# Kernel optimization log

Measured on AMD Instinct MI355X. Metric: run time of the kernel, lower is better.

Reference implementation:

```python
import jax, jax.numpy as jnp
import numpy as np

EPS = 1e-6

def _ln(x):
    mu = jnp.mean(x, -1, keepdims=True)
    var = jnp.mean((x - mu) ** 2, -1, keepdims=True)
    return (x - mu) / jnp.sqrt(var + EPS)

def _mha(q_in, k_in, v_in, w, mask, h):
    # w: [4, d, d] = (Wq, Wk, Wv, Wo), stored as [in, out]
    b, sq, d = q_in.shape
    dk = d // h
    q = (q_in @ w[0]).reshape(b, sq, h, dk)
    k = (k_in @ w[1]).reshape(b, k_in.shape[1], h, dk)
    v = (v_in @ w[2]).reshape(b, v_in.shape[1], h, dk)
    scores = jnp.einsum('bqhd,bkhd->bhqk', q, k) / np.sqrt(dk).astype(q.dtype)
    if mask is not None:
        scores = jnp.where(mask, scores, jnp.asarray(-jnp.inf, scores.dtype))
    attn = jax.nn.softmax(scores, -1)
    out = jnp.einsum('bhqk,bkhd->bqhd', attn, v).reshape(b, sq, d)
    return out @ w[3]

def setup_inputs() -> dict:
    B, S, D, V, NL, ML = 8, 256, 1024, 32000, 6, 256
    ks = jax.random.split(jax.random.key(0), 8)
    sc = 0.02
    return {
        'memory': jax.random.normal(ks[0], (B, S, D), jnp.float32),
        'gold_tokens': jax.random.randint(ks[1], (B, ML), 0, V),
        'attn_w': jax.random.normal(ks[2], (NL, 2, 4, D, D), jnp.float32) * sc,
        'ffn_w1': jax.random.normal(ks[3], (NL, D, 4 * D), jnp.float32) * sc,
        'ffn_w2': jax.random.normal(ks[4], (NL, 4 * D, D), jnp.float32) * sc,
        'tok_emb': jax.random.normal(ks[5], (V, D - ML), jnp.float32) * sc,
        'sos': jax.random.normal(ks[6], (D,), jnp.float32),
        'gen_w': jax.random.normal(ks[7], (D, V), jnp.float32) * sc,
    }

def reference(memory, gold_tokens, attn_w, ffn_w1, ffn_w2, tok_emb, sos, gen_w):
    B = memory.shape[0]
    ML = gold_tokens.shape[1]          # max_length == decoder len
    NL = attn_w.shape[0]
    H = 8
    temperature = 1.0
    # embedding: token embed (dim d-ML) concat one-hot position (dim ML)
    dec_input = gold_tokens[:, :-1]                      # [B, ML-1]
    tok = tok_emb[dec_input]                             # [B, ML-1, D-ML]
    pos = jax.nn.one_hot(jnp.arange(ML - 1), ML, dtype=tok.dtype)  # [ML-1, ML]
    pos = jnp.broadcast_to(pos[None], (B, ML - 1, ML))
    emb = jnp.concatenate([tok, pos], -1)                # [B, ML-1, D]
    sos_tok = jnp.broadcast_to(sos[None, None, :], (B, 1, sos.shape[0]))
    x = jnp.concatenate([sos_tok, emb], 1)               # [B, ML, D]
    causal = jnp.tril(jnp.ones((ML, ML), bool))[None, None]  # True = keep
    for l in range(NL):
        h1 = _ln(x)
        x = x + _mha(h1, h1, h1, attn_w[l, 0], causal, H)       # self-attn
        x = x + _mha(_ln(x), memory, memory, attn_w[l, 1], None, H)  # cross-attn (raw memory keys/values)
        h2 = _ln(x)
        x = x + jax.nn.relu(h2 @ ffn_w1[l]) @ ffn_w2[l]
    logits = _ln(x) @ gen_w
    return jax.nn.log_softmax(logits / temperature, -1)
```

## Files before the change

### kernel.cpp

```cpp
#include <hip/hip_runtime.h>
#include <hip/hip_bf16.h>
#include <cstdint>
#include <cstddef>

using bf16 = __hip_bfloat16;
typedef __attribute__((ext_vector_type(8))) short bf16x8;
typedef __attribute__((ext_vector_type(4))) float f32x4;

#define DEV static __device__ __forceinline__

DEV unsigned short f2bf(float f) {
    bf16 h = __float2bfloat16(f);
    return __builtin_bit_cast(unsigned short, h);
}

typedef const __attribute__((address_space(1))) void* as1cv;
typedef __attribute__((address_space(3))) void* as3v;

DEV void load_lds16(const void* g, void* l) {
    __builtin_amdgcn_global_load_lds((as1cv)g, (as3v)l, 16, 0, 0);
}

template<int EPI>
__global__ __launch_bounds__(256)
void gemm_k(const bf16* __restrict__ Ag, const bf16* __restrict__ Bg,
            void* __restrict__ Cg,
            int Mdim, int Ndim, int Kdim,
            int lda, int ldb, int ldc,
            int Hdim, long aZ1, long aZ2, long bZ1, long bZ2,
            long cZ1, long cZ2, float scale,
            float* __restrict__ pp, const bf16* __restrict__ Ag2, int ySplitA)
{
    __shared__ __align__(16) char lds[65536];

    const int t = threadIdx.x;
    const int wave = t >> 6, lane = t & 63;
    const int wr = wave >> 1, wc = wave & 1;
    const int lo = lane & 15, hi = lane >> 4;

    const int bx2 = blockIdx.x, by2 = blockIdx.y;
    const int m0 = bx2 * 128, n0 = by2 * 128;
    const int z = blockIdx.z;
    const int z1 = z / Hdim, z2 = z - z1 * Hdim;

    const bf16* Abase = (by2 >= ySplitA) ? Ag2 : Ag;
    const bf16* A = Abase + (size_t)z1 * aZ1 + (size_t)z2 * aZ2;
    const bf16* B = Bg + (size_t)z1 * bZ1 + (size_t)z2 * bZ2;

    f32x4 acc[4][4];
#pragma unroll
    for (int m = 0; m < 4; ++m)
#pragma unroll
        for (int n = 0; n < 4; ++n)
            acc[m][n] = f32x4{0.f, 0.f, 0.f, 0.f};

    const int nk = Kdim >> 6;

    auto stage = [&](int kt, int buf) {
        const int k0 = kt << 6;
        char* dA = lds + buf * 32768;
        char* dB = dA + 16384;
#pragma unroll
        for (int i = 0; i < 4; ++i) {
            int u = i * 256 + t;
            int row = u >> 3;
            int cb = (u & 7) ^ (row & 7);
            load_lds16(A + (size_t)(m0 + row) * lda + (k0 + cb * 8),
                       dA + i * 4096 + wave * 1024);
        }
#pragma unroll
        for (int i = 0; i < 4; ++i) {
            int u = i * 256 + t;
            int row = u >> 3;
            int cb = (u & 7) ^ (row & 7);
            load_lds16(B + (size_t)(n0 + row) * ldb + (k0 + cb * 8),
                       dB + i * 4096 + wave * 1024);
        }
    };

    stage(0, 0);
    int cur = 0;
    for (int kt = 0; kt < nk; ++kt) {
        __syncthreads();
        if (kt + 1 < nk) stage(kt + 1, cur ^ 1);
        char* ldsA = lds + cur * 32768;
        char* ldsB = ldsA + 16384;
#pragma unroll
        for (int kk = 0; kk < 2; ++kk) {
            bf16x8 af[4], bfr[4];
#pragma unroll
            for (int m = 0; m < 4; ++m) {
                int row = wr * 64 + m * 16 + lo;
                int cbyte = ((kk << 6) + (hi << 4)) ^ ((row & 7) << 4);
                af[m] = *(const bf16x8*)(ldsA + row * 128 + cbyte);
            }
#pragma unroll
            for (int n = 0; n < 4; ++n) {
                int row = wc * 64 + n * 16 + lo;
                int cbyte = ((kk << 6) + (hi << 4)) ^ ((row & 7) << 4);
                bfr[n] = *(const bf16x8*)(ldsB + row * 128 + cbyte);
            }
#pragma unroll
            for (int m = 0; m < 4; ++m)
#pragma unroll
                for (int n = 0; n < 4; ++n)
                    acc[m][n] = __builtin_amdgcn_mfma_f32_16x16x32_bf16(
                        af[m], bfr[n], acc[m][n], 0, 0, 0);
        }
        cur ^= 1;
    }

    const int rb = hi << 2;
    if (EPI == 0 || EPI == 1) {
        unsigned short* C = (unsigned short*)Cg + (size_t)z1 * cZ1 + (size_t)z2 * cZ2;
#pragma unroll
        for (int m = 0; m < 4; ++m)
#pragma unroll
            for (int n = 0; n < 4; ++n)
#pragma unroll
                for (int r = 0; r < 4; ++r) {
                    int row = m0 + wr * 64 + m * 16 + rb + r;
                    int col = n0 + wc * 64 + n * 16 + lo;
                    float v = acc[m][n][r];
                    if (EPI == 1) v = fmaxf(v, 0.f);
                    C[(size_t)row * ldc + col] = f2bf(v);
                }
    } else if (EPI == 5) {
        float* C = (float*)Cg + (size_t)z1 * cZ1 + (size_t)z2 * cZ2;
#pragma unroll
        for (int m = 0; m < 4; ++m)
#pragma unroll
            for (int n = 0; n < 4; ++n)
#pragma unroll
                for (int r = 0; r < 4; ++r) {
                    int row = m0 + wr * 64 + m * 16 + rb + r;
                    int col = n0 + wc * 64 + n * 16 + lo;
                    atomicAdd(&C[(size_t)row * ldc + col], acc[m][n][r]);
                }
    } else {
        float* C = (float*)Cg + (size_t)z1 * cZ1 + (size_t)z2 * cZ2;
#pragma unroll
        for (int m = 0; m < 4; ++m)
#pragma unroll
            for (int n = 0; n < 4; ++n)
#pragma unroll
                for (int r = 0; r < 4; ++r) {
                    int row = m0 + wr * 64 + m * 16 + rb + r;
                    int col = n0 + wc * 64 + n * 16 + lo;
                    float v = acc[m][n][r] * scale;
                    __builtin_nontemporal_store(v, &C[(size_t)row * ldc + col]);
                }
        __syncthreads();
        float* lp = (float*)lds;
#pragma unroll
        for (int m = 0; m < 4; ++m)
#pragma unroll
            for (int r = 0; r < 4; ++r) {
                float vm = -3.4e38f;
#pragma unroll
                for (int n = 0; n < 4; ++n) vm = fmaxf(vm, acc[m][n][r] * scale);
#pragma unroll
                for (int o = 1; o < 16; o <<= 1) vm = fmaxf(vm, __shfl_xor(vm, o));
                float vs = 0.f;
#pragma unroll
                for (int n = 0; n < 4; ++n) vs += __expf(acc[m][n][r] * scale - vm);
#pragma unroll
                for (int o = 1; o < 16; o <<= 1) vs += __shfl_xor(vs, o);
                if (lo == 0) {
                    int rl = wr * 64 + m * 16 + rb + r;
                    lp[(rl * 2 + wc) * 2 + 0] = vm;
                    lp[(rl * 2 + wc) * 2 + 1] = vs;
                }
            }
        __syncthreads();
        if (t < 128) {
            float ma = lp[(t * 2 + 0) * 2], sa = lp[(t * 2 + 0) * 2 + 1];
            float mb = lp[(t * 2 + 1) * 2], sb = lp[(t * 2 + 1) * 2 + 1];
            float mm = fmaxf(ma, mb);
            float ss = sa * __expf(ma - mm) + sb * __expf(mb - mm);
            size_t idx2 = ((size_t)(m0 + t) * gridDim.y + by2) * 2;
            pp[idx2] = mm; pp[idx2 + 1] = ss;
        }
    }
}

template<int CAUSAL>
__global__ __launch_bounds__(256)
void attn_k(const bf16* __restrict__ qkv, const bf16* __restrict__ VT,
            bf16* __restrict__ attno)
{
    __shared__ __align__(16) char ldsK[2][16384];
    __shared__ __align__(16) char ldsP[8192];
    const float SC = 0.088388347648318447f;

    const int t = threadIdx.x, w = t >> 6, lane = t & 63;
    const int lo = lane & 15, hi = lane >> 4;
    const int qb = blockIdx.x, z = blockIdx.y;
    const int b = z >> 3, h = z & 7;
    const int qr0 = qb * 64 + w * 16;

    const unsigned short* Qg = (const unsigned short*)qkv + (size_t)(b * 256) * 3072 + h * 128;
    const unsigned short* Kg = Qg + 1024;
    const unsigned short* VTz = (const unsigned short*)VT + (size_t)z * 32768;

    bf16x8 qf[4];
#pragma unroll
    for (int ks = 0; ks < 4; ++ks)
        qf[ks] = *(const bf16x8*)(Qg + (size_t)(qr0 + lo) * 3072 + ks * 32 + hi * 8);

    f32x4 accO[8];
#pragma unroll
    for (int n2 = 0; n2 < 8; ++n2) accO[n2] = f32x4{0.f, 0.f, 0.f, 0.f};
    float mrun[4], lrun[4];
#pragma unroll
    for (int r = 0; r < 4; ++r) { mrun[r] = -3.0e38f; lrun[r] = 0.f; }

    auto stageK = [&](int kt, int buf) {
#pragma unroll
        for (int i = 0; i < 4; ++i) {
            int u = i * 256 + t;
            int row = u >> 4, j = u & 15;
            int sj = (j & 8) | ((j ^ row) & 7);
            load_lds16(Kg + (size_t)(kt * 64 + row) * 3072 + sj * 8,
                       ldsK[buf] + i * 4096 + w * 1024);
        }
    };

    const int nkt = CAUSAL ? (qb + 1) : 4;
    stageK(0, 0);
    int cur = 0;
    for (int kt = 0; kt < nkt; ++kt) {
        __syncthreads();
        if (kt + 1 < nkt) stageK(kt + 1, cur ^ 1);

        f32x4 s4[4];
#pragma unroll
        for (int n = 0; n < 4; ++n) s4[n] = f32x4{0.f, 0.f, 0.f, 0.f};
#pragma unroll
        for (int ks = 0; ks < 4; ++ks)
#pragma unroll
            for (int n = 0; n < 4; ++n) {
                int kr = n * 16 + lo;
                int c = ks * 4 + hi;
                int sc2 = (c & 8) | ((c ^ (kr & 7)) & 7);
                bf16x8 kf = *(const bf16x8*)(ldsK[cur] + kr * 256 + sc2 * 16);
                s4[n] = __builtin_amdgcn_mfma_f32_16x16x32_bf16(qf[ks], kf, s4[n], 0, 0, 0);
            }

        float sv[4][4];
#pragma unroll
        for (int n = 0; n < 4; ++n)
#pragma unroll
            for (int r = 0; r < 4; ++r) {
                float v = s4[n][r] * SC;
                if (CAUSAL) {
                    int kg = kt * 64 + n * 16 + lo;
                    int qg2 = qb * 64 + w * 16 + hi * 4 + r;
                    if (kg > qg2) v = -3.0e38f;
                }
                sv[n][r] = v;
            }

        float sfv[4];
#pragma unroll
        for (int r = 0; r < 4; ++r) {
            float m2 = fmaxf(fmaxf(sv[0][r], sv[1][r]), fmaxf(sv[2][r], sv[3][r]));
#pragma unroll
            for (int o = 1; o < 16; o <<= 1) m2 = fmaxf(m2, __shfl_xor(m2, o));
            float mn = fmaxf(mrun[r], m2);
            sfv[r] = __expf(mrun[r] - mn);
            mrun[r] = mn;
        }
        float p[4][4], ts[4];
#pragma unroll
        for (int r = 0; r < 4; ++r) ts[r] = 0.f;
#pragma unroll
        for (int n = 0; n < 4; ++n)
#pragma unroll
            for (int r = 0; r < 4; ++r) {
                float e = __expf(sv[n][r] - mrun[r]);
                p[n][r] = e; ts[r] += e;
            }
#pragma unroll
        for (int r = 0; r < 4; ++r) {
            float s2 = ts[r];
#pragma unroll
            for (int o = 1; o < 16; o <<= 1) s2 += __shfl_xor(s2, o);
            lrun[r] = lrun[r] * sfv[r] + s2;
        }
#pragma unroll
        for (int n2 = 0; n2 < 8; ++n2)
#pragma unroll
            for (int r = 0; r < 4; ++r) accO[n2][r] *= sfv[r];

        char* pb = ldsP + w * 2048;
#pragma unroll
        for (int n = 0; n < 4; ++n)
#pragma unroll
            for (int r = 0; r < 4; ++r) {
                int q = hi * 4 + r, k = n * 16 + lo;
                int ch = (k >> 3) ^ (q & 7);
                *(unsigned short*)(pb + q * 128 + ch * 16 + (k & 7) * 2) = f2bf(p[n][r]);
            }

#pragma unroll
        for (int ks2 = 0; ks2 < 2; ++ks2) {
            int c2 = (ks2 * 4 + hi) ^ (lo & 7);
            bf16x8 pa = *(const bf16x8*)(pb + lo * 128 + c2 * 16);
#pragma unroll
            for (int n2 = 0; n2 < 8; ++n2) {
                int d = n2 * 16 + lo;
                bf16x8 vb = *(const bf16x8*)(VTz + (size_t)d * 256 + kt * 64 + ks2 * 32 + hi * 8);
                accO[n2] = __builtin_amdgcn_mfma_f32_16x16x32_bf16(pa, vb, accO[n2], 0, 0, 0);
            }
        }
        cur ^= 1;
    }

    float inv[4];
#pragma unroll
    for (int r = 0; r < 4; ++r) inv[r] = 1.f / lrun[r];
    unsigned short* Og = (unsigned short*)attno;
#pragma unroll
    for (int n2 = 0; n2 < 8; ++n2)
#pragma unroll
        for (int r = 0; r < 4; ++r) {
            int qg2 = qb * 64 + w * 16 + hi * 4 + r;
            int d = n2 * 16 + lo;
            Og[(size_t)(b * 256 + qg2) * 1024 + h * 128 + d] = f2bf(accO[n2][r] * inv[r]);
        }
}

DEV void wconv_tile(const float* __restrict__ W, unsigned short* __restrict__ WT,
                    int K, int N, int k0, int n0, int t, unsigned short* lds)
{
#pragma unroll
    for (int i = 0; i < 16; ++i) {
        int lin = i * 256 + t;
        int r = lin >> 6, c = lin & 63;
        float v = __builtin_nontemporal_load(&W[(size_t)(k0 + r) * N + n0 + c]);
        lds[c * 65 + r] = f2bf(v);
    }
    __syncthreads();
#pragma unroll
    for (int i = 0; i < 16; ++i) {
        int lin = i * 256 + t;
        int r = lin >> 6, c = lin & 63;
        WT[(size_t)(n0 + r) * K + k0 + c] = lds[r * 65 + c];
    }
}

__global__ __launch_bounds__(256)
void wconv_k(const float* __restrict__ W, bf16* __restrict__ WT, int K, int N)
{
    __shared__ unsigned short lds[64 * 65];
    size_t moff = (size_t)blockIdx.z * K * N;
    wconv_tile(W + moff, (unsigned short*)WT + moff, K, N,
               blockIdx.x * 64, blockIdx.y * 64, threadIdx.x, lds);
}

__global__ __launch_bounds__(256)
void wconv3_k(const float* __restrict__ Wa, const float* __restrict__ W1,
              const float* __restrict__ W2, bf16* __restrict__ WTa,
              bf16* __restrict__ WT1, bf16* __restrict__ WT2)
{
    __shared__ unsigned short lds[64 * 65];
    int bid = blockIdx.x, t = threadIdx.x;
    if (bid < 2048) {
        int mat = bid >> 8, r = bid & 255;
        size_t moff = (size_t)mat * 1048576;
        wconv_tile(Wa + moff, (unsigned short*)WTa + moff, 1024, 1024,
                   (r & 15) * 64, (r >> 4) * 64, t, lds);
    } else if (bid < 3072) {
        int idx = bid - 2048;
        wconv_tile(W1, (unsigned short*)WT1, 1024, 4096,
                   (idx & 15) * 64, (idx >> 4) * 64, t, lds);
    } else {
        int idx = bid - 3072;
        wconv_tile(W2, (unsigned short*)WT2, 4096, 1024,
                   (idx & 63) * 64, (idx >> 6) * 64, t, lds);
    }
}

__global__ __launch_bounds__(256)
void f2b_k(const float* __restrict__ in, bf16* __restrict__ out, int n4)
{
    int i = blockIdx.x * 256 + threadIdx.x;
    if (i >= n4) return;
    float4 v = ((const float4*)in)[i];
    ushort4 o;
    o.x = f2bf(v.x); o.y = f2bf(v.y); o.z = f2bf(v.z); o.w = f2bf(v.w);
    ((ushort4*)out)[i] = o;
}

__global__ __launch_bounds__(256)
void embed_k(const float* __restrict__ tok_emb, const int* __restrict__ gold,
             const float* __restrict__ sos, float* __restrict__ x)
{
    int row = blockIdx.x;
    int b = row >> 8, sq = row & 255;
    int c4 = threadIdx.x;
    float4 v;
    if (sq == 0) {
        v = ((const float4*)sos)[c4];
    } else {
        int c = c4 << 2;
        if (c < 768) {
            int tok = gold[b * 256 + sq - 1];
            v = ((const float4*)(tok_emb + (size_t)tok * 768))[c4];
        } else {
            int p = sq - 1;
            v.x = (c + 0 - 768 == p) ? 1.f : 0.f;
            v.y = (c + 1 - 768 == p) ? 1.f : 0.f;
            v.z = (c + 2 - 768 == p) ? 1.f : 0.f;
            v.w = (c + 3 - 768 == p) ? 1.f : 0.f;
        }
    }
    ((float4*)(x + (size_t)row * 1024))[c4] = v;
}

__global__ __launch_bounds__(256)
void ln_k(const float* __restrict__ x, bf16* __restrict__ out)
{
    int row = blockIdx.x;
    const float4* xr = (const float4*)(x + (size_t)row * 1024);
    float4 v = xr[threadIdx.x];
    float s = v.x + v.y + v.z + v.w;
    float ss = v.x * v.x + v.y * v.y + v.z * v.z + v.w * v.w;
    for (int o = 32; o > 0; o >>= 1) { s += __shfl_down(s, o); ss += __shfl_down(ss, o); }
    __shared__ float buf[8];
    int wv = threadIdx.x >> 6;
    if ((threadIdx.x & 63) == 0) { buf[wv] = s; buf[4 + wv] = ss; }
    __syncthreads();
    float S = buf[0] + buf[1] + buf[2] + buf[3];
    float SS = buf[4] + buf[5] + buf[6] + buf[7];
    float mean = S * (1.f / 1024.f);
    float var = SS * (1.f / 1024.f) - mean * mean;
    float rstd = rsqrtf(var + 1e-6f);
    ushort4 o;
    o.x = f2bf((v.x - mean) * rstd);
    o.y = f2bf((v.y - mean) * rstd);
    o.z = f2bf((v.z - mean) * rstd);
    o.w = f2bf((v.w - mean) * rstd);
    ((ushort4*)out)[(size_t)row * 256 + threadIdx.x] = o;
}

__global__ __launch_bounds__(256)
void vtrans_k(const bf16* __restrict__ v, bf16* __restrict__ VT)
{
    __shared__ unsigned short lds[128 * 65];
    int z = blockIdx.y;
    int b = z >> 3, hh = z & 7;
    int sc = blockIdx.x;
    const unsigned short* src = (const unsigned short*)v
        + (size_t)(b * 256 + sc * 64) * 3072 + hh * 128;
    int t = threadIdx.x;
#pragma unroll
    for (int i = 0; i < 32; ++i) {
        int lin = i * 256 + t;
        int sl = lin >> 7, d = lin & 127;
        lds[d * 65 + sl] = src[(size_t)sl * 3072 + d];
    }
    __syncthreads();
    unsigned short* dst = (unsigned short*)VT + (size_t)z * 32768 + sc * 64;
#pragma unroll
    for (int i = 0; i < 32; ++i) {
        int lin = i * 256 + t;
        int d = lin >> 6, sl = lin & 63;
        dst[(size_t)d * 256 + sl] = lds[d * 65 + sl];
    }
}

__global__ __launch_bounds__(256)
void lsesub_k(float* __restrict__ out, const float* __restrict__ pp)
{
    const int NB = 250;
    int row = blockIdx.x, t = threadIdx.x;
    float m = -3.4e38f, s = 0.f;
    if (t < NB) {
        m = pp[((size_t)row * NB + t) * 2];
        s = pp[((size_t)row * NB + t) * 2 + 1];
    }
    for (int o = 32; o > 0; o >>= 1) {
        float om = __shfl_down(m, o), os = __shfl_down(s, o);
        float nm = fmaxf(m, om);
        s = s * __expf(m - nm) + os * __expf(om - nm);
        m = nm;
    }
    __shared__ float bm[4], bs[4];
    __shared__ float sL;
    int wv = t >> 6;
    if ((t & 63) == 0) { bm[wv] = m; bs[wv] = s; }
    __syncthreads();
    if (t == 0) {
        float M = fmaxf(fmaxf(bm[0], bm[1]), fmaxf(bm[2], bm[3]));
        float S = bs[0] * __expf(bm[0] - M) + bs[1] * __expf(bm[1] - M)
                + bs[2] * __expf(bm[2] - M) + bs[3] * __expf(bm[3] - M);
        sL = M + logf(S);
    }
    __syncthreads();
    float L = sL;
    f32x4* p = (f32x4*)(out + (size_t)row * 32000);
    for (int i = t; i < 8000; i += 256) {
        f32x4 v = __builtin_nontemporal_load(&p[i]);
        v[0] -= L; v[1] -= L; v[2] -= L; v[3] -= L;
        __builtin_nontemporal_store(v, &p[i]);
    }
}

extern "C" void kernel_launch(void* const* d_in, const int* in_sizes, int n_in,
                              void* d_out, int out_size, void* d_ws, size_t ws_size,
                              hipStream_t stream)
{
    (void)in_sizes; (void)n_in; (void)out_size;
    const float* memory  = (const float*)d_in[0];
    const int*   gold    = (const int*)d_in[1];
    const float* attn_w  = (const float*)d_in[2];
    const float* ffn_w1  = (const float*)d_in[3];
    const float* ffn_w2  = (const float*)d_in[4];
    const float* tok_emb = (const float*)d_in[5];
    const float* sos     = (const float*)d_in[6];
    const float* gen_w   = (const float*)d_in[7];
    float* out = (float*)d_out;

    char* ws = (char*)d_ws;
    const size_t o_attnW = 0;
    const size_t o_ffn1W = o_attnW + 16777216;
    const size_t o_ffn2W = o_ffn1W + 8388608;
    const size_t o_qkv   = o_ffn2W + 8388608;
    const size_t o_attno = o_qkv + 12582912;
    const size_t o_tmp   = o_attno + 4194304;
    const size_t o_mem   = o_tmp + 29360128;
    const size_t o_x     = o_mem + 4194304;
    const size_t o_h     = o_x + 8388608;
    const size_t o_lse   = o_h + 4194304;
    const size_t NEEDED  = o_lse + 8192;
    if (ws_size < NEEDED) return;

    bf16*  attnWT = (bf16*)(ws + o_attnW);
    bf16*  ffn1WT = (bf16*)(ws + o_ffn1W);
    bf16*  ffn2WT = (bf16*)(ws + o_ffn2W);
    bf16*  qkv    = (bf16*)(ws + o_qkv);
    bf16*  attno  = (bf16*)(ws + o_attno);
    bf16*  VT     = (bf16*)(ws + o_tmp + 25165824);
    bf16*  ffnmid = (bf16*)(ws + o_tmp);
    bf16*  memb   = (bf16*)(ws + o_mem);
    float* x      = (float*)(ws + o_x);
    bf16*  h      = (bf16*)(ws + o_h);
    float* parts  = (float*)(ws + o_mem);
    bf16*  genWT  = (bf16*)(ws + 0);

    const int BIG = 1 << 30;

    f2b_k<<<2048, 256, 0, stream>>>(memory, memb, 2048 * 1024 / 4);
    embed_k<<<2048, 256, 0, stream>>>(tok_emb, gold, sos, x);

    for (int l = 0; l < 6; ++l) {
        wconv3_k<<<4096, 256, 0, stream>>>(attn_w + (size_t)l * 8388608,
            ffn_w1 + (size_t)l * 4194304, ffn_w2 + (size_t)l * 4194304,
            attnWT, ffn1WT, ffn2WT);

        ln_k<<<2048, 256, 0, stream>>>(x, h);
        gemm_k<0><<<dim3(16,24,1), 256, 0, stream>>>(h, attnWT, qkv,
            2048, 3072, 1024, 1024, 1024, 3072, 1, 0,0,0,0,0,0, 0.f, nullptr, nullptr, BIG);
        vtrans_k<<<dim3(4,64), 256, 0, stream>>>(qkv + 2048, VT);
        attn_k<1><<<dim3(4,64), 256, 0, stream>>>(qkv, VT, attno);
        gemm_k<5><<<dim3(16,8,2), 256, 0, stream>>>(attno, attnWT + 3 * 1048576, x,
            2048, 1024, 512, 1024, 1024, 1024, 2, 0,512, 0,512, 0,0, 0.f, nullptr, nullptr, BIG);

        ln_k<<<2048, 256, 0, stream>>>(x, h);
        gemm_k<0><<<dim3(16,24,1), 256, 0, stream>>>(h, attnWT + 4 * 1048576, qkv,
            2048, 3072, 1024, 1024, 1024, 3072, 1, 0,0,0,0,0,0, 0.f, nullptr, memb, 8);
        vtrans_k<<<dim3(4,64), 256, 0, stream>>>(qkv + 2048, VT);
        attn_k<0><<<dim3(4,64), 256, 0, stream>>>(qkv, VT, attno);
        gemm_k<5><<<dim3(16,8,2), 256, 0, stream>>>(attno, attnWT + 7 * 1048576, x,
            2048, 1024, 512, 1024, 1024, 1024, 2, 0,512, 0,512, 0,0, 0.f, nullptr, nullptr, BIG);

        ln_k<<<2048, 256, 0, stream>>>(x, h);
        gemm_k<1><<<dim3(16,32,1), 256, 0, stream>>>(h, ffn1WT, ffnmid,
            2048, 4096, 1024, 1024, 1024, 4096, 1, 0,0,0,0,0,0, 0.f, nullptr, nullptr, BIG);
        gemm_k<5><<<dim3(16,8,4), 256, 0, stream>>>(ffnmid, ffn2WT, x,
            2048, 1024, 1024, 4096, 4096, 1024, 4, 0,1024, 0,1024, 0,0, 0.f, nullptr, nullptr, BIG);
    }

    wconv_k<<<dim3(16,500,1), 256, 0, stream>>>(gen_w, genWT, 1024, 32000);
    ln_k<<<2048, 256, 0, stream>>>(x, h);
    gemm_k<4><<<dim3(16,250,1), 256, 0, stream>>>(h, genWT, out,
        2048, 32000, 1024, 1024, 1024, 32000, 1, 0,0,0,0,0,0, 1.f, parts, nullptr, BIG);
    lsesub_k<<<2048, 256, 0, stream>>>(out, parts);
}
```

Before: 1.657 ms.

## Add 256x256-tile GEMM kernel for vocab projection with fused LSE partials

```diff
diff --git a/kernel.cpp b/kernel.cpp
--- a/kernel.cpp
+++ b/kernel.cpp
@@ -125,7 +125,7 @@
                     if (EPI == 1) v = fmaxf(v, 0.f);
                     C[(size_t)row * ldc + col] = f2bf(v);
                 }
-    } else if (EPI == 5) {
+    } else {
         float* C = (float*)Cg + (size_t)z1 * cZ1 + (size_t)z2 * cZ2;
 #pragma unroll
         for (int m = 0; m < 4; ++m)
@@ -137,50 +137,139 @@
                     int col = n0 + wc * 64 + n * 16 + lo;
                     atomicAdd(&C[(size_t)row * ldc + col], acc[m][n][r]);
                 }
-    } else {
-        float* C = (float*)Cg + (size_t)z1 * cZ1 + (size_t)z2 * cZ2;
-#pragma unroll
-        for (int m = 0; m < 4; ++m)
-#pragma unroll
-            for (int n = 0; n < 4; ++n)
-#pragma unroll
-                for (int r = 0; r < 4; ++r) {
-                    int row = m0 + wr * 64 + m * 16 + rb + r;
-                    int col = n0 + wc * 64 + n * 16 + lo;
-                    float v = acc[m][n][r] * scale;
-                    __builtin_nontemporal_store(v, &C[(size_t)row * ldc + col]);
-                }
-        __syncthreads();
-        float* lp = (float*)lds;
-#pragma unroll
-        for (int m = 0; m < 4; ++m)
+    }
+}
+
+__global__ __launch_bounds__(512, 2)
+void gemm256_k(const bf16* __restrict__ Ag, const bf16* __restrict__ Bg,
+               float* __restrict__ Cg, int Kdim, int lda, int ldb, int ldc,
+               float* __restrict__ pp)
+{
+    __shared__ __align__(16) char lds[98304];
+
+    const int t = threadIdx.x;
+    const int wave = t >> 6, lane = t & 63;
+    const int wr = wave >> 2, wc = wave & 3;
+    const int lo = lane & 15, hi = lane >> 4;
+    const int m0 = blockIdx.x * 256, n0 = blockIdx.y * 256;
+
+    f32x4 acc[8][4];
+#pragma unroll
+    for (int m = 0; m < 8; ++m)
+#pragma unroll
+        for (int n = 0; n < 4; ++n)
+            acc[m][n] = f32x4{0.f, 0.f, 0.f, 0.f};
+
+    const int NT = Kdim >> 5;
+
+    auto stageOp = [&](const bf16* Op, int ld, int base0, int kt, char* dst) {
+#pragma unroll
+        for (int i = 0; i < 2; ++i) {
+            int u = i * 512 + t;
+            int row = u >> 2, j = u & 3;
+            int cb = j ^ (row & 3);
+            load_lds16(Op + (size_t)(base0 + row) * ld + (kt << 5) + cb * 8,
+                       dst + i * 8192 + wave * 1024);
+        }
+    };
+
+    stageOp(Ag, lda, m0, 0, lds);
+    stageOp(Bg, ldb, n0, 0, lds + 16384);
+    stageOp(Ag, lda, m0, 1, lds + 32768);
+    stageOp(Bg, ldb, n0, 1, lds + 32768 + 16384);
+
+    for (int kt = 0; kt < NT; ++kt) {
+        if (kt == NT - 1) asm volatile("s_waitcnt vmcnt(0)" ::: "memory");
+        else              asm volatile("s_waitcnt vmcnt(4)" ::: "memory");
+        __builtin_amdgcn_s_barrier();
+        __builtin_amdgcn_sched_barrier(0);
+
+        char* cA = lds + (kt % 3) * 32768;
+        char* cB = cA + 16384;
+        char* nA = lds + ((kt + 2) % 3) * 32768;
+
+        if (kt + 2 < NT) stageOp(Ag, lda, m0, kt + 2, nA);
+        bf16x8 bfr[4];
+#pragma unroll
+        for (int nf = 0; nf < 4; ++nf) {
+            int rb_ = wc * 64 + nf * 16 + lo;
+            bfr[nf] = *(const bf16x8*)(cB + rb_ * 64 + ((hi ^ (rb_ & 3)) << 4));
+        }
+        bf16x8 af[4];
+#pragma unroll
+        for (int mm = 0; mm < 4; ++mm) {
+            int ra = wr * 128 + mm * 16 + lo;
+            af[mm] = *(const bf16x8*)(cA + ra * 64 + ((hi ^ (ra & 3)) << 4));
+        }
+        __builtin_amdgcn_s_setprio(1);
+#pragma unroll
+        for (int mm = 0; mm < 4; ++mm)
+#pragma unroll
+            for (int nf = 0; nf < 4; ++nf)
+                acc[mm][nf] = __builtin_amdgcn_mfma_f32_16x16x32_bf16(
+                    af[mm], bfr[nf], acc[mm][nf], 0, 0, 0);
+        __builtin_amdgcn_s_setprio(0);
+
+        if (kt + 2 < NT) stageOp(Bg, ldb, n0, kt + 2, nA + 16384);
+#pragma unroll
+        for (int mm = 0; mm < 4; ++mm) {
+            int ra = wr * 128 + (4 + mm) * 16 + lo;
+            af[mm] = *(const bf16x8*)(cA + ra * 64 + ((hi ^ (ra & 3)) << 4));
+        }
+        __builtin_amdgcn_s_setprio(1);
+#pragma unroll
+        for (int mm = 0; mm < 4; ++mm)
+#pragma unroll
+            for (int nf = 0; nf < 4; ++nf)
+                acc[4 + mm][nf] = __builtin_amdgcn_mfma_f32_16x16x32_bf16(
+                    af[mm], bfr[nf], acc[4 + mm][nf], 0, 0, 0);
+        __builtin_amdgcn_s_setprio(0);
+    }
+
+#pragma unroll
+    for (int mf = 0; mf < 8; ++mf)
+#pragma unroll
+        for (int nf = 0; nf < 4; ++nf)
 #pragma unroll
             for (int r = 0; r < 4; ++r) {
-                float vm = -3.4e38f;
-#pragma unroll
-                for (int n = 0; n < 4; ++n) vm = fmaxf(vm, acc[m][n][r] * scale);
-#pragma unroll
-                for (int o = 1; o < 16; o <<= 1) vm = fmaxf(vm, __shfl_xor(vm, o));
-                float vs = 0.f;
-#pragma unroll
-                for (int n = 0; n < 4; ++n) vs += __expf(acc[m][n][r] * scale - vm);
-#pragma unroll
-                for (int o = 1; o < 16; o <<= 1) vs += __shfl_xor(vs, o);
-                if (lo == 0) {
-                    int rl = wr * 64 + m * 16 + rb + r;
-                    lp[(rl * 2 + wc) * 2 + 0] = vm;
-                    lp[(rl * 2 + wc) * 2 + 1] = vs;
-                }
-            }
-        __syncthreads();
-        if (t < 128) {
-            float ma = lp[(t * 2 + 0) * 2], sa = lp[(t * 2 + 0) * 2 + 1];
-            float mb = lp[(t * 2 + 1) * 2], sb = lp[(t * 2 + 1) * 2 + 1];
-            float mm = fmaxf(ma, mb);
-            float ss = sa * __expf(ma - mm) + sb * __expf(mb - mm);
-            size_t idx2 = ((size_t)(m0 + t) * gridDim.y + by2) * 2;
-            pp[idx2] = mm; pp[idx2 + 1] = ss;
-        }
+                int row = m0 + wr * 128 + mf * 16 + hi * 4 + r;
+                int col = n0 + wc * 64 + nf * 16 + lo;
+                __builtin_nontemporal_store(acc[mf][nf][r],
+                                            &Cg[(size_t)row * ldc + col]);
+            }
+    __syncthreads();
+    float* lp = (float*)lds;
+#pragma unroll
+    for (int mf = 0; mf < 8; ++mf)
+#pragma unroll
+        for (int r = 0; r < 4; ++r) {
+            float vm = fmaxf(fmaxf(acc[mf][0][r], acc[mf][1][r]),
+                             fmaxf(acc[mf][2][r], acc[mf][3][r]));
+#pragma unroll
+            for (int o = 1; o < 16; o <<= 1) vm = fmaxf(vm, __shfl_xor(vm, o));
+            float vs = 0.f;
+#pragma unroll
+            for (int nf = 0; nf < 4; ++nf) vs += __expf(acc[mf][nf][r] - vm);
+#pragma unroll
+            for (int o = 1; o < 16; o <<= 1) vs += __shfl_xor(vs, o);
+            if (lo == 0) {
+                int rl = wr * 128 + mf * 16 + hi * 4 + r;
+                lp[(rl * 4 + wc) * 2 + 0] = vm;
+                lp[(rl * 4 + wc) * 2 + 1] = vs;
+            }
+        }
+    __syncthreads();
+    if (t < 256) {
+        float mm = -3.4e38f, ss = 0.f;
+#pragma unroll
+        for (int w2 = 0; w2 < 4; ++w2) {
+            float m2 = lp[(t * 4 + w2) * 2], s2 = lp[(t * 4 + w2) * 2 + 1];
+            float nm = fmaxf(mm, m2);
+            ss = ss * __expf(mm - nm) + s2 * __expf(m2 - nm);
+            mm = nm;
+        }
+        size_t idx2 = ((size_t)(m0 + t) * gridDim.y + blockIdx.y) * 2;
+        pp[idx2] = mm; pp[idx2 + 1] = ss;
     }
 }
 
@@ -474,7 +563,7 @@
 __global__ __launch_bounds__(256)
 void lsesub_k(float* __restrict__ out, const float* __restrict__ pp)
 {
-    const int NB = 250;
+    const int NB = 125;
     int row = blockIdx.x, t = threadIdx.x;
     float m = -3.4e38f, s = 0.f;
     if (t < NB) {
@@ -585,7 +674,6 @@
 
     wconv_k<<<dim3(16,500,1), 256, 0, stream>>>(gen_w, genWT, 1024, 32000);
     ln_k<<<2048, 256, 0, stream>>>(x, h);
-    gemm_k<4><<<dim3(16,250,1), 256, 0, stream>>>(h, genWT, out,
-        2048, 32000, 1024, 1024, 1024, 32000, 1, 0,0,0,0,0,0, 1.f, parts, nullptr, BIG);
+    gemm256_k<<<dim3(8,125), 512, 0, stream>>>(h, genWT, out, 1024, 1024, 1024, 32000, parts);
     lsesub_k<<<2048, 256, 0, stream>>>(out, parts);
 }
```

Measured after the change: 1.667 ms. Within noise of the previous version (+0.6%).
